# Performance work log

Measured on AMD Instinct MI355X. Metric: run time of the kernel, lower is better.

The kernel has to match this reference:

```python
import jax, jax.numpy as jnp
import numpy as np

D_MODEL = 512
D_AUX = 64
B, N = 8, 2048


def setup_inputs() -> dict:
    key = jax.random.key(0)
    ks = jax.random.split(key, 12)
    lim = 1.0 / np.sqrt(D_MODEL)  # torch Linear default init scale
    inp = {
        "x": jax.random.normal(ks[0], (B, N, D_MODEL), dtype=jnp.float32),
        "query_aux": jax.random.normal(ks[1], (B, N, D_AUX), dtype=jnp.float32),
        "key_aux": jax.random.normal(ks[2], (B, N, D_AUX), dtype=jnp.float32),
        "adjacency_mask": jax.random.randint(ks[3], (B, N, N), 0, 2, dtype=jnp.int32),
        "merge_coefficients": jnp.float32(0.3),
        "Wq": jax.random.uniform(ks[4], (D_MODEL, D_MODEL), jnp.float32, -lim, lim),
        "bq": jax.random.uniform(ks[5], (D_MODEL,), jnp.float32, -lim, lim),
        "Wk": jax.random.uniform(ks[6], (D_MODEL, D_MODEL), jnp.float32, -lim, lim),
        "bk": jax.random.uniform(ks[7], (D_MODEL,), jnp.float32, -lim, lim),
        "Wv": jax.random.uniform(ks[8], (D_MODEL, D_MODEL), jnp.float32, -lim, lim),
        "bv": jax.random.uniform(ks[9], (D_MODEL,), jnp.float32, -lim, lim),
        "threshold": jnp.float32(0.5),
    }
    return inp


def reference(x, query_aux, key_aux, adjacency_mask, merge_coefficients,
              Wq, bq, Wk, bk, Wv, bv, threshold):
    d_model = x.shape[-1]
    d_aux = key_aux.shape[-1]
    scale = jnp.asarray(d_model, x.dtype) ** 0.5
    scale_aux = jnp.asarray(d_aux, x.dtype) ** 0.5

    q = x @ Wq.T + bq  # [B,N,D]
    k = x @ Wk.T + bk
    v = x @ Wv.T + bv

    scores = jnp.einsum('bnd,bmd->bnm', q, k) / scale  # [B,N,N]
    scores_aux = jnp.einsum('bnd,bmd->bnm', query_aux, key_aux) / scale_aux

    # data-dependent merge: where aux score nonzero AND score above learned threshold
    merge_mask = (scores_aux != 0) & (scores > threshold)
    merged = (1.0 - merge_coefficients) * scores + merge_coefficients * scores_aux
    scores = jnp.where(merge_mask, merged, scores)

    mask_value = jnp.finfo(scores.dtype).min
    scores = jnp.where(adjacency_mask == 0, mask_value, scores)

    weights = jax.nn.softmax(scores, axis=-1)
    return jnp.einsum('bnm,bmd->bnd', weights, v)
```

## Files before the change

kernel.cpp:

```cpp
#include <hip/hip_runtime.h>
#include <cstdint>

#define SEQ    2048
#define DM     512
#define DAUX   64

typedef _Float16 f16;
typedef __attribute__((ext_vector_type(2))) _Float16 f16x2;
typedef __attribute__((ext_vector_type(4))) _Float16 f16x4;
typedef __attribute__((ext_vector_type(8))) _Float16 f16x8;
typedef __attribute__((ext_vector_type(4))) float fx4;
typedef __attribute__((ext_vector_type(16))) float fx16;

__device__ __forceinline__ void g2l16(const void* g, void* l) {
  __builtin_amdgcn_global_load_lds(
      (__attribute__((address_space(1))) void*)const_cast<void*>(g),
      (__attribute__((address_space(3))) void*)l, 16, 0, 0);
}

__device__ __forceinline__ void stage32(const f16* __restrict__ g0, int stride,
                                        f16* lds, int t) {
#pragma unroll
  for (int p = 0; p < 2; ++p) {
    int L = p * 256 + t;
    int row = L >> 2;
    int jp = L & 3;
    int jl = jp ^ ((row >> 1) & 3);
    g2l16(g0 + (size_t)row * stride + jl * 8, lds + L * 8);
  }
}
__device__ __forceinline__ f16x8 frag32(const f16* lds, int row, int kq) {
  int jp = (kq >> 3) ^ ((row >> 1) & 3);
  return *(const f16x8*)(lds + row * 32 + jp * 8);
}

__device__ __forceinline__ void stage64(const f16* __restrict__ g0, int stride,
                                        f16* lds, int t) {
#pragma unroll
  for (int p = 0; p < 4; ++p) {
    int L = p * 256 + t;
    int row = L >> 3;
    int jp = L & 7;
    int jl = jp ^ (row & 7);
    g2l16(g0 + (size_t)row * stride + jl * 8, lds + L * 8);
  }
}
__device__ __forceinline__ f16x8 frag64(const f16* lds, int row, int kq) {
  int jp = (kq >> 3) ^ (row & 7);
  return *(const f16x8*)(lds + row * 64 + jp * 8);
}

__device__ __forceinline__ void chunk3_32(const f16* Ah, const f16* Al,
                                          const f16* Bh, const f16* Bl,
                                          fx16 acc[2][2], int wm, int wn, int lane) {
  const int r31 = lane & 31;
  const int kq = (lane >> 5) * 8;
#pragma unroll
  for (int k0 = 0; k0 < 32; k0 += 16) {
    f16x8 ah[2], al[2];
#pragma unroll
    for (int it = 0; it < 2; ++it) {
      int row = wm * 64 + it * 32 + r31;
      ah[it] = frag32(Ah, row, k0 + kq);
      al[it] = frag32(Al, row, k0 + kq);
    }
#pragma unroll
    for (int jt = 0; jt < 2; ++jt) {
      int col = wn * 64 + jt * 32 + r31;
      f16x8 bh = frag32(Bh, col, k0 + kq);
      f16x8 bl = frag32(Bl, col, k0 + kq);
#pragma unroll
      for (int it = 0; it < 2; ++it) {
        acc[it][jt] = __builtin_amdgcn_mfma_f32_32x32x16_f16(ah[it], bh, acc[it][jt], 0, 0, 0);
        acc[it][jt] = __builtin_amdgcn_mfma_f32_32x32x16_f16(ah[it], bl, acc[it][jt], 0, 0, 0);
        acc[it][jt] = __builtin_amdgcn_mfma_f32_32x32x16_f16(al[it], bh, acc[it][jt], 0, 0, 0);
      }
    }
  }
}

__device__ __forceinline__ void chunk1_64(const f16* A, const f16* B,
                                          fx16 acc[2][2], int wm, int wn, int lane) {
  const int r31 = lane & 31;
  const int kq = (lane >> 5) * 8;
#pragma unroll
  for (int k0 = 0; k0 < 64; k0 += 16) {
    f16x8 a[2];
#pragma unroll
    for (int it = 0; it < 2; ++it)
      a[it] = frag64(A, wm * 64 + it * 32 + r31, k0 + kq);
#pragma unroll
    for (int jt = 0; jt < 2; ++jt) {
      f16x8 b = frag64(B, wn * 64 + jt * 32 + r31, k0 + kq);
#pragma unroll
      for (int it = 0; it < 2; ++it)
        acc[it][jt] = __builtin_amdgcn_mfma_f32_32x32x16_f16(a[it], b, acc[it][jt], 0, 0, 0);
    }
  }
}

__global__ __launch_bounds__(256) void convert_split(
    const float* __restrict__ x, const float* __restrict__ Wq,
    const float* __restrict__ Wk, const float* __restrict__ Wv,
    f16* __restrict__ xh, f16* __restrict__ xl,
    f16* __restrict__ Wh, f16* __restrict__ Wl) {
  int idx = blockIdx.x * 256 + threadIdx.x;
  const float* src; f16* dh; f16* dl; size_t off;
  if (idx < 2097152) { src = x; off = (size_t)idx; dh = xh; dl = xl; }
  else {
    int rr = idx - 2097152;
    int w = rr >> 16, o = rr & 65535;
    src = (w == 0) ? Wq : (w == 1) ? Wk : Wv;
    off = (size_t)o;
    dh = Wh + (size_t)w * 262144; dl = Wl + (size_t)w * 262144;
  }
  float4 v = ((const float4*)src)[off];
  float vv[4] = {v.x, v.y, v.z, v.w};
  f16x4 hv, lv;
#pragma unroll
  for (int i = 0; i < 4; ++i) {
    float s = vv[i] * 32.0f;
    f16 hi = (f16)s;
    hv[i] = hi;
    lv[i] = (f16)(s - (float)hi);
  }
  *(f16x4*)(dh + off * 4) = hv;
  *(f16x4*)(dl + off * 4) = lv;
}

__global__ __launch_bounds__(256) void qkv_mfma(
    const f16* __restrict__ xh, const f16* __restrict__ xl,
    const f16* __restrict__ Wh, const f16* __restrict__ Wl,
    const float* __restrict__ bq, const float* __restrict__ bk, const float* __restrict__ bv,
    f16* __restrict__ qh, f16* __restrict__ ql,
    f16* __restrict__ kh, f16* __restrict__ kl,
    f16* __restrict__ vt) {
  __shared__ __align__(16) f16 sm[16384];
  const int t = threadIdx.x;
  const int i0 = blockIdx.x * 128, j0 = blockIdx.y * 128, z = blockIdx.z;
  const f16* WhZ = Wh + (size_t)z * 262144;
  const f16* WlZ = Wl + (size_t)z * 262144;
  const int lane = t & 63, wave = t >> 6;
  const int wm = wave >> 1, wn = wave & 1;
  const int r31 = lane & 31, half = lane >> 5;
  fx16 acc[2][2] = {};
  if (z < 2) {
    f16 *Ah = sm, *Al = sm + 4096, *Bh = sm + 8192, *Bl = sm + 12288;
    for (int d0 = 0; d0 < DM; d0 += 32) {
      __syncthreads();
      stage32(xh + (size_t)i0 * DM + d0, DM, Ah, t);
      stage32(xl + (size_t)i0 * DM + d0, DM, Al, t);
      stage32(WhZ + (size_t)j0 * DM + d0, DM, Bh, t);
      stage32(WlZ + (size_t)j0 * DM + d0, DM, Bl, t);
      __syncthreads();
      chunk3_32(Ah, Al, Bh, Bl, acc, wm, wn, lane);
    }
  } else {
    f16 *Ah = sm, *Bh = sm + 8192;
    for (int d0 = 0; d0 < DM; d0 += 64) {
      __syncthreads();
      stage64(xh + (size_t)i0 * DM + d0, DM, Ah, t);
      stage64(WhZ + (size_t)j0 * DM + d0, DM, Bh, t);
      __syncthreads();
      chunk1_64(Ah, Bh, acc, wm, wn, lane);
    }
  }
  const float* bias = (z == 0) ? bq : (z == 1) ? bk : bv;
  if (z < 2) {
    f16* oh = z ? kh : qh;  f16* ol = z ? kl : ql;
#pragma unroll
    for (int it = 0; it < 2; ++it)
#pragma unroll
      for (int jt = 0; jt < 2; ++jt) {
        int j = j0 + wn * 64 + jt * 32 + r31;
        float bj = bias[j];
#pragma unroll
        for (int r = 0; r < 16; ++r) {
          int ib = i0 + wm * 64 + it * 32 + (r & 3) + 8 * (r >> 2) + 4 * half;
          float val = acc[it][jt][r] * (1.0f / 1024.0f) + bj;
          float s = val * 32.0f;
          f16 hi = (f16)s;
          oh[(size_t)ib * DM + j] = hi;
          ol[(size_t)ib * DM + j] = (f16)(s - (float)hi);
        }
      }
  } else {
#pragma unroll
    for (int it = 0; it < 2; ++it)
#pragma unroll
      for (int jt = 0; jt < 2; ++jt) {
        int j = j0 + wn * 64 + jt * 32 + r31;
        float bj = bias[j];
#pragma unroll
        for (int q4 = 0; q4 < 4; ++q4) {
          int ib = i0 + wm * 64 + it * 32 + 8 * q4 + 4 * half;
          int bb = ib >> 11, nb = ib & 2047;
          f16x4 hv;
#pragma unroll
          for (int g = 0; g < 4; ++g)
            hv[g] = (f16)(acc[it][jt][q4 * 4 + g] * (1.0f / 1024.0f) + bj);
          *(f16x4*)(vt + ((size_t)(bb * DM + j)) * SEQ + nb) = hv;
        }
      }
  }
}

__global__ __launch_bounds__(256) void scores_mfma(
    const f16* __restrict__ qh, const f16* __restrict__ ql,
    const f16* __restrict__ kh, const f16* __restrict__ kl,
    const float* __restrict__ qa, const float* __restrict__ ka,
    const int* __restrict__ adj,
    const float* __restrict__ mc_p, const float* __restrict__ thr_p,
    f16* __restrict__ S16) {
  __shared__ __align__(16) f16 sm[16384];
  f16 *Ah = sm, *Al = sm + 4096, *Bh = sm + 8192, *Bl = sm + 12288;
  f16 *QAl = sm;
  f16 *KAl = sm + 8192;
  const int t = threadIdx.x;
  const int n0 = blockIdx.x * 128, m0 = blockIdx.y * 128, b = blockIdx.z;
  const int lane = t & 63, wave = t >> 6;
  const int wm = wave >> 1, wn = wave & 1;
  const int r31 = lane & 31, half = lane >> 5;
  const int kq = half * 8;

  const float* QAb = qa + ((size_t)b * SEQ + n0) * DAUX;
  const float* KAb = ka + ((size_t)b * SEQ + m0) * DAUX;
#pragma unroll
  for (int p = 0; p < 4; ++p) {
    int L8 = p * 256 + t;
    int row = L8 >> 3, jb = L8 & 7;
    int c8 = jb * 8;
    int jp = jb ^ (row & 7);
    float4 u0 = *(const float4*)(QAb + (size_t)row * DAUX + c8);
    float4 u1 = *(const float4*)(QAb + (size_t)row * DAUX + c8 + 4);
    f16x8 hq = {(f16)u0.x,(f16)u0.y,(f16)u0.z,(f16)u0.w,(f16)u1.x,(f16)u1.y,(f16)u1.z,(f16)u1.w};
    *(f16x8*)(QAl + row * 64 + jp * 8) = hq;
    float4 w0 = *(const float4*)(KAb + (size_t)row * DAUX + c8);
    float4 w1 = *(const float4*)(KAb + (size_t)row * DAUX + c8 + 4);
    f16x8 hk = {(f16)w0.x,(f16)w0.y,(f16)w0.z,(f16)w0.w,(f16)w1.x,(f16)w1.y,(f16)w1.z,(f16)w1.w};
    *(f16x8*)(KAl + row * 64 + jp * 8) = hk;
  }
  __syncthreads();
  f16x2 sax2[2][2][8];
  {
    fx16 aacc[2][2] = {};
#pragma unroll
    for (int k0 = 0; k0 < 64; k0 += 16) {
      f16x8 qaf[2];
#pragma unroll
      for (int it = 0; it < 2; ++it)
        qaf[it] = frag64(QAl, wm * 64 + it * 32 + r31, k0 + kq);
#pragma unroll
      for (int jt = 0; jt < 2; ++jt) {
        f16x8 kaf = frag64(KAl, wn * 64 + jt * 32 + r31, k0 + kq);
#pragma unroll
        for (int it = 0; it < 2; ++it)
          aacc[it][jt] = __builtin_amdgcn_mfma_f32_32x32x16_f16(qaf[it], kaf, aacc[it][jt], 0, 0, 0);
      }
    }
#pragma unroll
    for (int it = 0; it < 2; ++it)
#pragma unroll
      for (int jt = 0; jt < 2; ++jt)
#pragma unroll
        for (int r = 0; r < 16; ++r)
          sax2[it][jt][r >> 1][r & 1] = (f16)aacc[it][jt][r];
  }
  fx16 acc[2][2] = {};
  const f16* qhB = qh + ((size_t)b * SEQ + n0) * DM;
  const f16* qlB = ql + ((size_t)b * SEQ + n0) * DM;
  const f16* khB = kh + ((size_t)b * SEQ + m0) * DM;
  const f16* klB = kl + ((size_t)b * SEQ + m0) * DM;
  for (int d0 = 0; d0 < DM; d0 += 32) {
    __syncthreads();
    stage32(qhB + d0, DM, Ah, t);
    stage32(qlB + d0, DM, Al, t);
    stage32(khB + d0, DM, Bh, t);
    stage32(klB + d0, DM, Bl, t);
    __syncthreads();
    chunk3_32(Ah, Al, Bh, Bl, acc, wm, wn, lane);
  }
  const float mc = *mc_p, thr = *thr_p;
  const float invC = 1.0f / (1024.0f * 22.62741699796952f);
#pragma unroll
  for (int it = 0; it < 2; ++it)
#pragma unroll
    for (int jt = 0; jt < 2; ++jt) {
      int col = m0 + wn * 64 + jt * 32 + r31;
#pragma unroll
      for (int r = 0; r < 16; ++r) {
        int row = n0 + wm * 64 + it * 32 + (r & 3) + 8 * (r >> 2) + 4 * half;
        size_t rbase = ((size_t)b * SEQ + row) * SEQ;
        float s = acc[it][jt][r] * invC;
        float sa = (float)sax2[it][jt][r >> 1][r & 1] * 0.125f;
        if (sa != 0.0f && s > thr) s = (1.0f - mc) * s + mc * sa;
        if (adj[rbase + col] == 0) s = -65504.0f;
        S16[rbase + col] = (f16)s;
      }
    }
}

__global__ __launch_bounds__(256) void softmax_p(
    f16* __restrict__ S16, float* __restrict__ rowsum) {
  const size_t row = blockIdx.x;
  f16* Sr = S16 + row * SEQ;
  const int t = threadIdx.x;
  f16x8 v = *(const f16x8*)(Sr + t * 8);
  float vals[8];
#pragma unroll
  for (int i = 0; i < 8; ++i) vals[i] = (float)v[i];
  float m = vals[0];
#pragma unroll
  for (int i = 1; i < 8; ++i) m = fmaxf(m, vals[i]);
#pragma unroll
  for (int off = 32; off >= 1; off >>= 1) m = fmaxf(m, __shfl_down(m, off, 64));
  __shared__ float wred[4];
  __shared__ float bmax;
  const int wv = t >> 6, ln = t & 63;
  if (ln == 0) wred[wv] = m;
  __syncthreads();
  if (t == 0) bmax = fmaxf(fmaxf(wred[0], wred[1]), fmaxf(wred[2], wred[3]));
  __syncthreads();
  const float mm = bmax;
  f16x8 p16;
  float z = 0.f;
#pragma unroll
  for (int i = 0; i < 8; ++i) {
    f16 p = (f16)(__expf(vals[i] - mm) * 1024.0f);
    p16[i] = p;
    z += (float)p;
  }
#pragma unroll
  for (int off = 32; off >= 1; off >>= 1) z += __shfl_down(z, off, 64);
  __syncthreads();
  if (ln == 0) wred[wv] = z;
  __syncthreads();
  if (t == 0) rowsum[row] = wred[0] + wred[1] + wred[2] + wred[3];
  *(f16x8*)(Sr + t * 8) = p16;
}

__global__ __launch_bounds__(256) void pv_mfma(
    const f16* __restrict__ P16, const f16* __restrict__ vt,
    const float* __restrict__ rowsum, float* __restrict__ O) {
  __shared__ __align__(16) f16 sm[16384];
  f16 *Ps = sm, *Vs = sm + 8192;
  const int t = threadIdx.x;
  const int n0 = blockIdx.x * 128, d0 = blockIdx.y * 128, b = blockIdx.z;
  const int lane = t & 63, wave = t >> 6;
  const int wm = wave >> 1, wn = wave & 1;
  const int r31 = lane & 31, half = lane >> 5;
  fx16 acc[2][2] = {};
  const f16* Pb = P16 + ((size_t)b * SEQ + n0) * SEQ;
  const f16* Vb = vt + ((size_t)b * DM + d0) * SEQ;
  for (int m0 = 0; m0 < SEQ; m0 += 64) {
    __syncthreads();
    stage64(Pb + m0, SEQ, Ps, t);
    stage64(Vb + m0, SEQ, Vs, t);
    __syncthreads();
    chunk1_64(Ps, Vs, acc, wm, wn, lane);
  }
#pragma unroll
  for (int it = 0; it < 2; ++it)
#pragma unroll
    for (int jt = 0; jt < 2; ++jt) {
      int d = d0 + wn * 64 + jt * 32 + r31;
#pragma unroll
      for (int r = 0; r < 16; ++r) {
        int n = n0 + wm * 64 + it * 32 + (r & 3) + 8 * (r >> 2) + 4 * half;
        float inv = 1.0f / rowsum[(size_t)b * SEQ + n];
        O[((size_t)b * SEQ + n) * DM + d] = acc[it][jt][r] * inv;
      }
    }
}

extern "C" void kernel_launch(void* const* d_in, const int* in_sizes, int n_in,
                              void* d_out, int out_size, void* d_ws, size_t ws_size,
                              hipStream_t stream) {
  const float* x   = (const float*)d_in[0];
  const float* qa  = (const float*)d_in[1];
  const float* ka  = (const float*)d_in[2];
  const int*   adj = (const int*)d_in[3];
  const float* mc  = (const float*)d_in[4];
  const float* Wq  = (const float*)d_in[5];
  const float* bq  = (const float*)d_in[6];
  const float* Wk  = (const float*)d_in[7];
  const float* bk  = (const float*)d_in[8];
  const float* Wv  = (const float*)d_in[9];
  const float* bv  = (const float*)d_in[10];
  const float* thr = (const float*)d_in[11];
  float* out = (float*)d_out;

  f16* qh  = (f16*)d_ws;
  f16* ql  = qh + 8388608;
  f16* kh  = ql + 8388608;
  f16* kl  = kh + 8388608;
  f16* vt  = kl + 8388608;
  f16* S16 = vt + 8388608;
  float* rowsum = (float*)(S16 + 33554432);
  f16* xh = S16;
  f16* xl = xh + 8388608;
  f16* Wh = xl + 8388608;
  f16* Wl = Wh + 786432;

  convert_split<<<8960, 256, 0, stream>>>(x, Wq, Wk, Wv, xh, xl, Wh, Wl);
  qkv_mfma<<<dim3(128, 4, 3), 256, 0, stream>>>(xh, xl, Wh, Wl, bq, bk, bv,
                                                qh, ql, kh, kl, vt);
  scores_mfma<<<dim3(16, 16, 8), 256, 0, stream>>>(qh, ql, kh, kl, qa, ka, adj,
                                                   mc, thr, S16);
  softmax_p<<<16384, 256, 0, stream>>>(S16, rowsum);
  pv_mfma<<<dim3(16, 4, 8), 256, 0, stream>>>(S16, vt, rowsum, out);
}
```

Baseline: 506.8 us.

## Double-buffer LDS staging in GEMM kernels and use wave-per-row softmax

Doubles LDS to 64KB in the qkv, scores and pv kernels so the next K-chunk's global-to-LDS loads are issued before the MFMAs on the current chunk, with one barrier per iteration instead of two. The scores kernel also prefetches the first Q/K chunk while converting the auxiliary tensors. Softmax now gives each row to one wavefront with shuffle-xor reductions, dropping the shared-memory block reductions and barriers. The larger LDS footprint may lower occupancy per CU.

New measurement: 502.4 us. Within noise of the previous version (-0.9%).

```diff
diff --git a/kernel.cpp b/kernel.cpp
--- a/kernel.cpp
+++ b/kernel.cpp
@@ -135,7 +135,7 @@
     f16* __restrict__ qh, f16* __restrict__ ql,
     f16* __restrict__ kh, f16* __restrict__ kl,
     f16* __restrict__ vt) {
-  __shared__ __align__(16) f16 sm[16384];
+  __shared__ __align__(16) f16 sm[32768];
   const int t = threadIdx.x;
   const int i0 = blockIdx.x * 128, j0 = blockIdx.y * 128, z = blockIdx.z;
   const f16* WhZ = Wh + (size_t)z * 262144;
@@ -144,25 +144,43 @@
   const int wm = wave >> 1, wn = wave & 1;
   const int r31 = lane & 31, half = lane >> 5;
   fx16 acc[2][2] = {};
+  const f16* xhB = xh + (size_t)i0 * DM;
+  const f16* xlB = xl + (size_t)i0 * DM;
+  const f16* WhB = WhZ + (size_t)j0 * DM;
+  const f16* WlB = WlZ + (size_t)j0 * DM;
   if (z < 2) {
-    f16 *Ah = sm, *Al = sm + 4096, *Bh = sm + 8192, *Bl = sm + 12288;
-    for (int d0 = 0; d0 < DM; d0 += 32) {
-      __syncthreads();
-      stage32(xh + (size_t)i0 * DM + d0, DM, Ah, t);
-      stage32(xl + (size_t)i0 * DM + d0, DM, Al, t);
-      stage32(WhZ + (size_t)j0 * DM + d0, DM, Bh, t);
-      stage32(WlZ + (size_t)j0 * DM + d0, DM, Bl, t);
-      __syncthreads();
-      chunk3_32(Ah, Al, Bh, Bl, acc, wm, wn, lane);
+    stage32(xhB, DM, sm, t);
+    stage32(xlB, DM, sm + 4096, t);
+    stage32(WhB, DM, sm + 8192, t);
+    stage32(WlB, DM, sm + 12288, t);
+    __syncthreads();
+    for (int c = 0; c < 16; ++c) {
+      f16* cur = sm + (c & 1) * 16384;
+      if (c < 15) {
+        f16* nxt = sm + ((c + 1) & 1) * 16384;
+        int d0 = (c + 1) * 32;
+        stage32(xhB + d0, DM, nxt, t);
+        stage32(xlB + d0, DM, nxt + 4096, t);
+        stage32(WhB + d0, DM, nxt + 8192, t);
+        stage32(WlB + d0, DM, nxt + 12288, t);
+      }
+      chunk3_32(cur, cur + 4096, cur + 8192, cur + 12288, acc, wm, wn, lane);
+      if (c < 15) __syncthreads();
     }
   } else {
-    f16 *Ah = sm, *Bh = sm + 8192;
-    for (int d0 = 0; d0 < DM; d0 += 64) {
-      __syncthreads();
-      stage64(xh + (size_t)i0 * DM + d0, DM, Ah, t);
-      stage64(WhZ + (size_t)j0 * DM + d0, DM, Bh, t);
-      __syncthreads();
-      chunk1_64(Ah, Bh, acc, wm, wn, lane);
+    stage64(xhB, DM, sm, t);
+    stage64(WhB, DM, sm + 8192, t);
+    __syncthreads();
+    for (int c = 0; c < 8; ++c) {
+      f16* cur = sm + (c & 1) * 16384;
+      if (c < 7) {
+        f16* nxt = sm + ((c + 1) & 1) * 16384;
+        int d0 = (c + 1) * 64;
+        stage64(xhB + d0, DM, nxt, t);
+        stage64(WhB + d0, DM, nxt + 8192, t);
+      }
+      chunk1_64(cur, cur + 8192, acc, wm, wn, lane);
+      if (c < 7) __syncthreads();
     }
   }
   const float* bias = (z == 0) ? bq : (z == 1) ? bk : bv;
@@ -212,10 +230,7 @@
     const int* __restrict__ adj,
     const float* __restrict__ mc_p, const float* __restrict__ thr_p,
     f16* __restrict__ S16) {
-  __shared__ __align__(16) f16 sm[16384];
-  f16 *Ah = sm, *Al = sm + 4096, *Bh = sm + 8192, *Bl = sm + 12288;
-  f16 *QAl = sm;
-  f16 *KAl = sm + 8192;
+  __shared__ __align__(16) f16 sm[32768];
   const int t = threadIdx.x;
   const int n0 = blockIdx.x * 128, m0 = blockIdx.y * 128, b = blockIdx.z;
   const int lane = t & 63, wave = t >> 6;
@@ -223,6 +238,18 @@
   const int r31 = lane & 31, half = lane >> 5;
   const int kq = half * 8;
 
+  const f16* qhB = qh + ((size_t)b * SEQ + n0) * DM;
+  const f16* qlB = ql + ((size_t)b * SEQ + n0) * DM;
+  const f16* khB = kh + ((size_t)b * SEQ + m0) * DM;
+  const f16* klB = kl + ((size_t)b * SEQ + m0) * DM;
+
+  stage32(qhB, DM, sm, t);
+  stage32(qlB, DM, sm + 4096, t);
+  stage32(khB, DM, sm + 8192, t);
+  stage32(klB, DM, sm + 12288, t);
+
+  f16* QAl = sm + 16384;
+  f16* KAl = sm + 24576;
   const float* QAb = qa + ((size_t)b * SEQ + n0) * DAUX;
   const float* KAb = ka + ((size_t)b * SEQ + m0) * DAUX;
 #pragma unroll
@@ -241,6 +268,7 @@
     *(f16x8*)(KAl + row * 64 + jp * 8) = hk;
   }
   __syncthreads();
+
   f16x2 sax2[2][2][8];
   {
     fx16 aacc[2][2] = {};
@@ -266,20 +294,23 @@
         for (int r = 0; r < 16; ++r)
           sax2[it][jt][r >> 1][r & 1] = (f16)aacc[it][jt][r];
   }
+  __syncthreads();
+
   fx16 acc[2][2] = {};
-  const f16* qhB = qh + ((size_t)b * SEQ + n0) * DM;
-  const f16* qlB = ql + ((size_t)b * SEQ + n0) * DM;
-  const f16* khB = kh + ((size_t)b * SEQ + m0) * DM;
-  const f16* klB = kl + ((size_t)b * SEQ + m0) * DM;
-  for (int d0 = 0; d0 < DM; d0 += 32) {
-    __syncthreads();
-    stage32(qhB + d0, DM, Ah, t);
-    stage32(qlB + d0, DM, Al, t);
-    stage32(khB + d0, DM, Bh, t);
-    stage32(klB + d0, DM, Bl, t);
-    __syncthreads();
-    chunk3_32(Ah, Al, Bh, Bl, acc, wm, wn, lane);
-  }
+  for (int c = 0; c < 16; ++c) {
+    f16* cur = sm + (c & 1) * 16384;
+    if (c < 15) {
+      f16* nxt = sm + ((c + 1) & 1) * 16384;
+      int d0 = (c + 1) * 32;
+      stage32(qhB + d0, DM, nxt, t);
+      stage32(qlB + d0, DM, nxt + 4096, t);
+      stage32(khB + d0, DM, nxt + 8192, t);
+      stage32(klB + d0, DM, nxt + 12288, t);
+    }
+    chunk3_32(cur, cur + 4096, cur + 8192, cur + 12288, acc, wm, wn, lane);
+    if (c < 15) __syncthreads();
+  }
+
   const float mc = *mc_p, thr = *thr_p;
   const float invC = 1.0f / (1024.0f * 22.62741699796952f);
 #pragma unroll
@@ -302,48 +333,44 @@
 
 __global__ __launch_bounds__(256) void softmax_p(
     f16* __restrict__ S16, float* __restrict__ rowsum) {
-  const size_t row = blockIdx.x;
+  const int wv = threadIdx.x >> 6, ln = threadIdx.x & 63;
+  const size_t row = (size_t)blockIdx.x * 4 + wv;
   f16* Sr = S16 + row * SEQ;
-  const int t = threadIdx.x;
-  f16x8 v = *(const f16x8*)(Sr + t * 8);
-  float vals[8];
-#pragma unroll
-  for (int i = 0; i < 8; ++i) vals[i] = (float)v[i];
+  f16x8 v[4];
+  float vals[32];
+#pragma unroll
+  for (int j = 0; j < 4; ++j) {
+    v[j] = *(const f16x8*)(Sr + j * 512 + ln * 8);
+#pragma unroll
+    for (int i = 0; i < 8; ++i) vals[j * 8 + i] = (float)v[j][i];
+  }
   float m = vals[0];
 #pragma unroll
-  for (int i = 1; i < 8; ++i) m = fmaxf(m, vals[i]);
-#pragma unroll
-  for (int off = 32; off >= 1; off >>= 1) m = fmaxf(m, __shfl_down(m, off, 64));
-  __shared__ float wred[4];
-  __shared__ float bmax;
-  const int wv = t >> 6, ln = t & 63;
-  if (ln == 0) wred[wv] = m;
-  __syncthreads();
-  if (t == 0) bmax = fmaxf(fmaxf(wred[0], wred[1]), fmaxf(wred[2], wred[3]));
-  __syncthreads();
-  const float mm = bmax;
-  f16x8 p16;
+  for (int i = 1; i < 32; ++i) m = fmaxf(m, vals[i]);
+#pragma unroll
+  for (int off = 1; off < 64; off <<= 1) m = fmaxf(m, __shfl_xor(m, off, 64));
   float z = 0.f;
-#pragma unroll
-  for (int i = 0; i < 8; ++i) {
-    f16 p = (f16)(__expf(vals[i] - mm) * 1024.0f);
-    p16[i] = p;
-    z += (float)p;
-  }
-#pragma unroll
-  for (int off = 32; off >= 1; off >>= 1) z += __shfl_down(z, off, 64);
-  __syncthreads();
-  if (ln == 0) wred[wv] = z;
-  __syncthreads();
-  if (t == 0) rowsum[row] = wred[0] + wred[1] + wred[2] + wred[3];
-  *(f16x8*)(Sr + t * 8) = p16;
+  f16x8 p16[4];
+#pragma unroll
+  for (int j = 0; j < 4; ++j)
+#pragma unroll
+    for (int i = 0; i < 8; ++i) {
+      f16 p = (f16)(__expf(vals[j * 8 + i] - m) * 1024.0f);
+      p16[j][i] = p;
+      z += (float)p;
+    }
+#pragma unroll
+  for (int off = 1; off < 64; off <<= 1) z += __shfl_xor(z, off, 64);
+  if (ln == 0) rowsum[row] = z;
+#pragma unroll
+  for (int j = 0; j < 4; ++j)
+    *(f16x8*)(Sr + j * 512 + ln * 8) = p16[j];
 }
 
 __global__ __launch_bounds__(256) void pv_mfma(
     const f16* __restrict__ P16, const f16* __restrict__ vt,
     const float* __restrict__ rowsum, float* __restrict__ O) {
-  __shared__ __align__(16) f16 sm[16384];
-  f16 *Ps = sm, *Vs = sm + 8192;
+  __shared__ __align__(16) f16 sm[32768];
   const int t = threadIdx.x;
   const int n0 = blockIdx.x * 128, d0 = blockIdx.y * 128, b = blockIdx.z;
   const int lane = t & 63, wave = t >> 6;
@@ -352,12 +379,19 @@
   fx16 acc[2][2] = {};
   const f16* Pb = P16 + ((size_t)b * SEQ + n0) * SEQ;
   const f16* Vb = vt + ((size_t)b * DM + d0) * SEQ;
-  for (int m0 = 0; m0 < SEQ; m0 += 64) {
-    __syncthreads();
-    stage64(Pb + m0, SEQ, Ps, t);
-    stage64(Vb + m0, SEQ, Vs, t);
-    __syncthreads();
-    chunk1_64(Ps, Vs, acc, wm, wn, lane);
+  stage64(Pb, SEQ, sm, t);
+  stage64(Vb, SEQ, sm + 8192, t);
+  __syncthreads();
+  for (int c = 0; c < 32; ++c) {
+    f16* cur = sm + (c & 1) * 16384;
+    if (c < 31) {
+      f16* nxt = sm + ((c + 1) & 1) * 16384;
+      int m0 = (c + 1) * 64;
+      stage64(Pb + m0, SEQ, nxt, t);
+      stage64(Vb + m0, SEQ, nxt + 8192, t);
+    }
+    chunk1_64(cur, cur + 8192, acc, wm, wn, lane);
+    if (c < 31) __syncthreads();
   }
 #pragma unroll
   for (int it = 0; it < 2; ++it)
@@ -407,6 +441,6 @@
                                                 qh, ql, kh, kl, vt);
   scores_mfma<<<dim3(16, 16, 8), 256, 0, stream>>>(qh, ql, kh, kl, qa, ka, adj,
                                                    mc, thr, S16);
-  softmax_p<<<16384, 256, 0, stream>>>(S16, rowsum);
+  softmax_p<<<4096, 256, 0, stream>>>(S16, rowsum);
   pv_mfma<<<dim3(16, 4, 8), 256, 0, stream>>>(S16, vt, rowsum, out);
 }
```
